# Optimization experiments

Hardware: AMD Instinct MI355X
Metric: run time of the kernel (lower is better)

## Reference

```python
import jax, jax.numpy as jnp
import numpy as np

S, B, D, H, FF, L, V, O = 512, 32, 512, 8, 2048, 6, 32000, 1000
DH = D // H
EPS = 1e-5


def layer_norm(x, g, b):
    mu = jnp.mean(x, axis=-1, keepdims=True)
    var = jnp.mean((x - mu) ** 2, axis=-1, keepdims=True)
    return (x - mu) * jax.lax.rsqrt(var + EPS) * g + b


def positional_encoding(seq_len, dim):
    pos = np.arange(seq_len, dtype=np.float32)[:, None]
    i = np.arange(dim)
    angle = pos / (10000.0 ** ((i // 2 * 2.0) / dim))
    pe = np.where(i % 2 == 0, np.sin(angle), np.cos(angle)).astype(np.float32)
    return jnp.asarray(pe)  # [seq_len, dim]


def setup_inputs() -> dict:
    key = jax.random.key(0)
    ks = jax.random.split(key, 16)
    sc = 0.02
    inp = {
        'x': jax.random.randint(ks[0], (S, B), 0, V, dtype=jnp.int32),
        'x_len': jnp.full((B,), S, dtype=jnp.int32),
        'emb': jax.random.normal(ks[1], (V, D), jnp.float32) * sc,
        'Wq': jax.random.normal(ks[2], (L, D, D), jnp.float32) * sc,
        'bq': jnp.zeros((L, D), jnp.float32),
        'Wk': jax.random.normal(ks[3], (L, D, D), jnp.float32) * sc,
        'bk': jnp.zeros((L, D), jnp.float32),
        'Wv': jax.random.normal(ks[4], (L, D, D), jnp.float32) * sc,
        'bv': jnp.zeros((L, D), jnp.float32),
        'Wo': jax.random.normal(ks[5], (L, D, D), jnp.float32) * sc,
        'bo': jnp.zeros((L, D), jnp.float32),
        'ln1_g': jnp.ones((L, D), jnp.float32),
        'ln1_b': jnp.zeros((L, D), jnp.float32),
        'W1': jax.random.normal(ks[6], (L, D, FF), jnp.float32) * sc,
        'b1': jnp.zeros((L, FF), jnp.float32),
        'W2': jax.random.normal(ks[7], (L, FF, D), jnp.float32) * sc,
        'b2': jnp.zeros((L, D), jnp.float32),
        'ln2_g': jnp.ones((L, D), jnp.float32),
        'ln2_b': jnp.zeros((L, D), jnp.float32),
        'W_fc': jax.random.normal(ks[8], (S * D, O), jnp.float32) * sc,
        'b_fc': jnp.zeros((O,), jnp.float32),
    }
    return inp


def reference(x, x_len, emb, Wq, bq, Wk, bk, Wv, bv, Wo, bo, ln1_g, ln1_b,
              W1, b1, W2, b2, ln2_g, ln2_b, W_fc, b_fc):
    out = emb[x]                      # [S, B, D]
    out = jnp.transpose(out, (1, 0, 2))  # [B, S, D]
    out = out + positional_encoding(S, D)[None, :, :]
    scale = DH ** -0.5
    for l in range(L):
        # NOTE: faithful to the original buggy head-split: plain row-major
        # reshape [B,S,D] -> [B*H,S,DH] without a [B,H,S,DH] transpose.
        q = jnp.reshape(out @ Wq[l] + bq[l], (B * H, S, DH))
        k = jnp.reshape(out @ Wk[l] + bk[l], (B * H, S, DH))
        v = jnp.reshape(out @ Wv[l] + bv[l], (B * H, S, DH))
        attn = jax.nn.softmax(jnp.einsum('gqd,gkd->gqk', q, k) * scale, axis=-1)
        ctx = jnp.einsum('gqk,gkd->gqd', attn, v).reshape(B, S, D)
        h = layer_norm(ctx @ Wo[l] + bo[l] + out, ln1_g[l], ln1_b[l])
        f = jax.nn.relu(h @ W1[l] + b1[l]) @ W2[l] + b2[l]
        out = layer_norm(f + h, ln2_g[l], ln2_b[l])
    out = out.reshape(B, S * D)
    return out @ W_fc + b_fc          # [B, O]
```

## Files before the change

kernel.cpp:

```cpp
#include <hip/hip_runtime.h>
#include <cstdint>
#include <cstddef>

#define S_  512
#define B_  32
#define D_  512
#define FF_ 2048
#define L_  6
#define O_  1000
#define M_  (B_*S_)
#define G_  256
#define DH_ 64

typedef __attribute__((ext_vector_type(8))) short bf16x8;
typedef __attribute__((ext_vector_type(4))) float f32x4;
typedef __attribute__((ext_vector_type(16))) float f32x16;

__device__ __forceinline__ unsigned short f2bf(float f) {
  unsigned int u = __builtin_bit_cast(unsigned int, f);
  u = (u + 0x7fffu + ((u >> 16) & 1u)) >> 16;
  return (unsigned short)u;
}
__device__ __forceinline__ float bf2f(unsigned short u) {
  return __builtin_bit_cast(float, (unsigned int)u << 16);
}
__device__ __forceinline__ unsigned int pkbf(float a, float b) {
  return (unsigned int)f2bf(a) | ((unsigned int)f2bf(b) << 16);
}
__device__ __forceinline__ unsigned int prm(float a, float b) {
  return __builtin_amdgcn_perm(__builtin_bit_cast(unsigned int, b),
                               __builtin_bit_cast(unsigned int, a), 0x07060302u);
}
__device__ __forceinline__ void gload_lds16(const void* g, void* l) {
  __builtin_amdgcn_global_load_lds(
      (const __attribute__((address_space(1))) unsigned int*)g,
      (__attribute__((address_space(3))) unsigned int*)l, 16, 0, 0);
}

__global__ void pe_kernel(float* __restrict__ pe) {
  int i = blockIdx.x * 256 + threadIdx.x;
  int s = i >> 9, d = i & 511;
  double de = (double)(d & ~1);
  double ang = (double)s * exp(de * (-9.210340371976184 / 512.0));
  pe[i] = (d & 1) ? (float)cos(ang) : (float)sin(ang);
}

__global__ void wconv_kernel(const float* __restrict__ W, unsigned short* __restrict__ Wt,
                             int K, int N, size_t ozs) {
  __shared__ float tile[32][33];
  const float* Wl = W + (size_t)blockIdx.z * K * N;
  unsigned short* Wtl = Wt + (size_t)blockIdx.z * ozs;
  int k0 = blockIdx.x * 32, n0 = blockIdx.y * 32;
  int c = threadIdx.x & 31, rb = threadIdx.x >> 5;
#pragma unroll
  for (int i = 0; i < 4; ++i) {
    int r = rb + i * 8;
    tile[r][c] = Wl[(size_t)(k0 + r) * N + n0 + c];
  }
  __syncthreads();
#pragma unroll
  for (int i = 0; i < 4; ++i) {
    int r = rb + i * 8;
    Wtl[(size_t)(n0 + r) * K + k0 + c] = f2bf(tile[c][r]);
  }
}

__global__ void embed_kernel(const int* __restrict__ x, const float* __restrict__ emb,
                             const float* __restrict__ pe, unsigned short* __restrict__ xb) {
  int bi = blockIdx.x;
  int s = bi / B_, b = bi % B_;
  int tok = x[s * B_ + b];
  int d = threadIdx.x * 4;
  float4 e = *(const float4*)(emb + (size_t)tok * D_ + d);
  float4 p = *(const float4*)(pe + (size_t)s * D_ + d);
  size_t o = ((size_t)b * S_ + s) * D_ + d;
  ushort4 u;
  u.x = f2bf(e.x + p.x); u.y = f2bf(e.y + p.y);
  u.z = f2bf(e.z + p.z); u.w = f2bf(e.w + p.w);
  *(ushort4*)(xb + o) = u;
}

__global__ __launch_bounds__(256, 2) void gemm_kernel(
    const unsigned short* __restrict__ A, const unsigned short* __restrict__ Bt,
    const float* __restrict__ bias, unsigned short* __restrict__ outb,
    int K, int N, int relu, int nbx) {
  __shared__ unsigned short As[3][128 * 32];
  __shared__ unsigned short Bs[3][256 * 32];
  int nwg = nbx * (M_ / 128);
  int cpx = nwg >> 3;
  int id = blockIdx.x;
  int wg = (id & 7) * cpx + (id >> 3);
  int bx = wg % nbx, by = wg / nbx;
  int m0 = by * 128, n0 = bx * 256;

  int tid = threadIdx.x, lane = tid & 63, wid = tid >> 6;
  f32x4 acc[8][4];
#pragma unroll
  for (int mi = 0; mi < 8; ++mi)
#pragma unroll
    for (int ni = 0; ni < 4; ++ni) acc[mi][ni] = (f32x4)0.0f;

  int srow = lane >> 2, scol = (lane & 3) * 8;
  const unsigned short* Abase = A + (size_t)m0 * K;
  const unsigned short* Bbase = Bt + (size_t)n0 * K;
  int c16 = lane & 15, hi = lane >> 4;
  int koff = hi * 8;
  int brow = wid * 64 + c16;
  int nk = K >> 5;

  auto STAGE = [&](int kt, int bb) {
    int k0 = kt * 32;
#pragma unroll
    for (int i = 0; i < 6; ++i) {
      int c = wid * 6 + i;
      if (c < 8) {
        gload_lds16(Abase + (size_t)(c * 16 + srow) * K + k0 + scol, (char*)As[bb] + c * 1024);
      } else {
        int c2 = c - 8;
        gload_lds16(Bbase + (size_t)(c2 * 16 + srow) * K + k0 + scol, (char*)Bs[bb] + c2 * 1024);
      }
    }
  };

  STAGE(0, 0); STAGE(1, 1); STAGE(2, 2);
  int bb = 0;
  for (int kt = 0; kt < nk; ++kt) {
    int rem = nk - 1 - kt;
    if (rem >= 2)      asm volatile("s_waitcnt vmcnt(12)" ::: "memory");
    else if (rem == 1) asm volatile("s_waitcnt vmcnt(6)" ::: "memory");
    else               asm volatile("s_waitcnt vmcnt(0)" ::: "memory");
    __builtin_amdgcn_s_barrier();
    __builtin_amdgcn_sched_barrier(0);
    bf16x8 af[8], bfr[4];
#pragma unroll
    for (int mi = 0; mi < 8; ++mi) af[mi] = *(const bf16x8*)&As[bb][(mi * 16 + c16) * 32 + koff];
#pragma unroll
    for (int ni = 0; ni < 4; ++ni) bfr[ni] = *(const bf16x8*)&Bs[bb][(brow + ni * 16) * 32 + koff];
    __builtin_amdgcn_s_setprio(1);
#pragma unroll
    for (int mi = 0; mi < 8; ++mi)
#pragma unroll
      for (int ni = 0; ni < 4; ++ni)
        acc[mi][ni] = __builtin_amdgcn_mfma_f32_16x16x32_bf16(bfr[ni], af[mi], acc[mi][ni], 0, 0, 0);
    __builtin_amdgcn_s_setprio(0);
    __builtin_amdgcn_sched_barrier(0);
    __builtin_amdgcn_s_barrier();
    if (kt + 3 < nk) STAGE(kt + 3, bb);
    bb = (bb == 2) ? 0 : bb + 1;
  }

#pragma unroll
  for (int ni = 0; ni < 4; ++ni) {
    int colb = n0 + wid * 64 + ni * 16 + hi * 4;
    float4 bv = *(const float4*)(bias + colb);
#pragma unroll
    for (int mi = 0; mi < 8; ++mi) {
      int row = m0 + mi * 16 + c16;
      float v0 = acc[mi][ni][0] + bv.x;
      float v1 = acc[mi][ni][1] + bv.y;
      float v2 = acc[mi][ni][2] + bv.z;
      float v3 = acc[mi][ni][3] + bv.w;
      if (relu) { v0 = fmaxf(v0, 0.f); v1 = fmaxf(v1, 0.f); v2 = fmaxf(v2, 0.f); v3 = fmaxf(v3, 0.f); }
      *(uint2*)(outb + (size_t)row * N + colb) = make_uint2(pkbf(v0, v1), pkbf(v2, v3));
    }
  }
}

__global__ __launch_bounds__(256, 3) void gemm128_kernel(
    const unsigned short* __restrict__ A, const unsigned short* __restrict__ Bt,
    const float* __restrict__ b0, const float* __restrict__ b1, const float* __restrict__ b2,
    unsigned short* __restrict__ o0, unsigned short* __restrict__ o1, unsigned short* __restrict__ o2,
    int K, int N, int relu, int split, int nbx) {
  __shared__ unsigned short As[2][128 * 32];
  __shared__ unsigned short Bs[2][128 * 32];
  int nwg = nbx * (M_ / 128);
  int cpx = nwg >> 3;
  int id = blockIdx.x;
  int wg = (id & 7) * cpx + (id >> 3);
  int bx = wg % nbx, by = wg / nbx;
  int m0 = by * 128, n0 = bx * 128;

  int tid = threadIdx.x, lane = tid & 63, wid = tid >> 6;
  int wm = wid >> 1, wn = wid & 1;
  f32x4 acc[4][4];
#pragma unroll
  for (int mi = 0; mi < 4; ++mi)
#pragma unroll
    for (int ni = 0; ni < 4; ++ni) acc[mi][ni] = (f32x4)0.0f;

  int srow = lane >> 2, scol = (lane & 3) * 8;
  const unsigned short* Abase = A + (size_t)m0 * K;
  const unsigned short* Bbase = Bt + (size_t)n0 * K;
  int c16 = lane & 15, hi = lane >> 4;
  int koff = hi * 8;
  int arow = wm * 64 + c16, brow = wn * 64 + c16;
  int nk = K >> 5;

  auto STAGE = [&](int kt, int bb) {
    int k0 = kt * 32;
#pragma unroll
    for (int i = 0; i < 2; ++i) {
      int c = wid * 2 + i;
      gload_lds16(Abase + (size_t)(c * 16 + srow) * K + k0 + scol, (char*)As[bb] + c * 1024);
      gload_lds16(Bbase + (size_t)(c * 16 + srow) * K + k0 + scol, (char*)Bs[bb] + c * 1024);
    }
  };

  STAGE(0, 0); STAGE(1, 1);
  int bb = 0;
  for (int kt = 0; kt < nk; ++kt) {
    if (kt + 1 < nk) asm volatile("s_waitcnt vmcnt(4)" ::: "memory");
    else             asm volatile("s_waitcnt vmcnt(0)" ::: "memory");
    __builtin_amdgcn_s_barrier();
    __builtin_amdgcn_sched_barrier(0);
    bf16x8 af[4], bfr[4];
#pragma unroll
    for (int mi = 0; mi < 4; ++mi) af[mi] = *(const bf16x8*)&As[bb][(arow + mi * 16) * 32 + koff];
#pragma unroll
    for (int ni = 0; ni < 4; ++ni) bfr[ni] = *(const bf16x8*)&Bs[bb][(brow + ni * 16) * 32 + koff];
    __builtin_amdgcn_s_setprio(1);
#pragma unroll
    for (int mi = 0; mi < 4; ++mi)
#pragma unroll
      for (int ni = 0; ni < 4; ++ni)
        acc[mi][ni] = __builtin_amdgcn_mfma_f32_16x16x32_bf16(bfr[ni], af[mi], acc[mi][ni], 0, 0, 0);
    __builtin_amdgcn_s_setprio(0);
    __builtin_amdgcn_sched_barrier(0);
    __builtin_amdgcn_s_barrier();
    if (kt + 2 < nk) STAGE(kt + 2, bb);
    bb ^= 1;
  }

  const float* bias = b0;
  unsigned short* outb = o0;
  int nbase = n0, ostride = N;
  if (split) {
    int seg = n0 >> 9;
    if (seg == 1) { bias = b1; outb = o1; }
    else if (seg == 2) { bias = b2; outb = o2; }
    nbase = n0 & 511; ostride = 512;
  }
#pragma unroll
  for (int ni = 0; ni < 4; ++ni) {
    int colb = nbase + wn * 64 + ni * 16 + hi * 4;
    float4 bv = *(const float4*)(bias + colb);
#pragma unroll
    for (int mi = 0; mi < 4; ++mi) {
      int row = m0 + wm * 64 + mi * 16 + c16;
      float v0 = acc[mi][ni][0] + bv.x;
      float v1 = acc[mi][ni][1] + bv.y;
      float v2 = acc[mi][ni][2] + bv.z;
      float v3 = acc[mi][ni][3] + bv.w;
      if (relu) { v0 = fmaxf(v0, 0.f); v1 = fmaxf(v1, 0.f); v2 = fmaxf(v2, 0.f); v3 = fmaxf(v3, 0.f); }
      *(uint2*)(outb + (size_t)row * ostride + colb) = make_uint2(pkbf(v0, v1), pkbf(v2, v3));
    }
  }
}

__global__ __launch_bounds__(128) void addln_kernel(
    const unsigned short* __restrict__ Y, const unsigned short* __restrict__ R,
    const float* __restrict__ g, const float* __restrict__ b,
    unsigned short* __restrict__ Out) {
  __shared__ float red[2], red2[2];
  int row = blockIdx.x, t = threadIdx.x;
  size_t o = (size_t)row * 512 + t * 4;
  ushort4 yv = *(const ushort4*)(Y + o);
  ushort4 rv = *(const ushort4*)(R + o);
  float v0 = bf2f(yv.x) + bf2f(rv.x);
  float v1 = bf2f(yv.y) + bf2f(rv.y);
  float v2 = bf2f(yv.z) + bf2f(rv.z);
  float v3 = bf2f(yv.w) + bf2f(rv.w);
  float s = v0 + v1 + v2 + v3;
#pragma unroll
  for (int m = 1; m < 64; m <<= 1) s += __shfl_xor(s, m);
  if ((t & 63) == 0) red[t >> 6] = s;
  __syncthreads();
  float mean = (red[0] + red[1]) * (1.0f / 512.0f);
  float d0 = v0 - mean, d1 = v1 - mean, d2 = v2 - mean, d3 = v3 - mean;
  float sq = d0 * d0 + d1 * d1 + d2 * d2 + d3 * d3;
#pragma unroll
  for (int m = 1; m < 64; m <<= 1) sq += __shfl_xor(sq, m);
  if ((t & 63) == 0) red2[t >> 6] = sq;
  __syncthreads();
  float var = (red2[0] + red2[1]) * (1.0f / 512.0f);
  float rstd = rsqrtf(var + 1e-5f);
  float4 gg = *(const float4*)(g + t * 4);
  float4 bb = *(const float4*)(b + t * 4);
  float y0 = d0 * rstd * gg.x + bb.x;
  float y1 = d1 * rstd * gg.y + bb.y;
  float y2 = d2 * rstd * gg.z + bb.z;
  float y3 = d3 * rstd * gg.w + bb.w;
  *(uint2*)(Out + o) = make_uint2(pkbf(y0, y1), pkbf(y2, y3));
}

__global__ __launch_bounds__(256) void attn_kernel(
    const unsigned short* __restrict__ Q, const unsigned short* __restrict__ Kb,
    const unsigned short* __restrict__ Vb, unsigned short* __restrict__ Ctx) {
  __shared__ char KlB[8192];
  __shared__ char VtB[8192];
  int g = blockIdx.y;
  int q0 = blockIdx.x * 256;
  const unsigned short* Kg = Kb + (size_t)g * 512 * 64;
  const unsigned short* Vg = Vb + (size_t)g * 512 * 64;
  int tid = threadIdx.x, lane = tid & 63, wid = tid >> 6;
  int l31 = lane & 31, h = lane >> 5;
  bool lo = (lane < 32);
  int qrowA = q0 + wid * 64 + l31;
  int qrowB = qrowA + 32;
  const float sc2 = 0.125f * 1.44269504f;

  bf16x8 qfa[4], qfb[4];
  {
    const unsigned short* qpa = Q + ((size_t)g * 512 + qrowA) * 64;
    const unsigned short* qpb = Q + ((size_t)g * 512 + qrowB) * 64;
#pragma unroll
    for (int c = 0; c < 4; ++c) {
      bf16x8 ra = *(const bf16x8*)(qpa + c * 16 + h * 8);
      bf16x8 rb = *(const bf16x8*)(qpb + c * 16 + h * 8);
      union { unsigned int u[4]; bf16x8 v; } ua, ub;
#pragma unroll
      for (int j = 0; j < 4; ++j) {
        ua.u[j] = pkbf(bf2f((unsigned short)ra[2 * j]) * sc2,
                       bf2f((unsigned short)ra[2 * j + 1]) * sc2);
        ub.u[j] = pkbf(bf2f((unsigned short)rb[2 * j]) * sc2,
                       bf2f((unsigned short)rb[2 * j + 1]) * sc2);
      }
      qfa[c] = ua.v; qfb[c] = ub.v;
    }
  }

  f32x16 cA0 = (f32x16)0.0f, cA1 = (f32x16)0.0f;
  f32x16 cB0 = (f32x16)0.0f, cB1 = (f32x16)0.0f;
  float mrA = -3.0e38f, lsA = 0.0f;
  float mrB = -3.0e38f, lsB = 0.0f;

  int rowS = tid >> 2;
  int cbA = (tid & 3) * 16;
  int cbB = cbA + 64;
  int swA = cbA ^ ((rowS & 7) << 4);
  int swB = cbB ^ ((rowS & 7) << 4);

  bf16x8 kc0 = *(const bf16x8*)(Kg + (size_t)rowS * 64 + cbA / 2);
  bf16x8 kc1 = *(const bf16x8*)(Kg + (size_t)rowS * 64 + cbB / 2);
  bf16x8 vc0 = *(const bf16x8*)(Vg + (size_t)rowS * 64 + cbA / 2);
  bf16x8 vc1 = *(const bf16x8*)(Vg + (size_t)rowS * 64 + cbB / 2);

  for (int kt = 0; kt < 8; ++kt) {
    __syncthreads();
    *(bf16x8*)(KlB + rowS * 128 + swA) = kc0;
    *(bf16x8*)(KlB + rowS * 128 + swB) = kc1;
#pragma unroll
    for (int j = 0; j < 8; ++j) {
      int dA = cbA / 2 + j;
      int dB = cbB / 2 + j;
      *(unsigned short*)(VtB + dA * 128 + ((2 * rowS) ^ ((dA & 7) << 4))) = (unsigned short)vc0[j];
      *(unsigned short*)(VtB + dB * 128 + ((2 * rowS) ^ ((dB & 7) << 4))) = (unsigned short)vc1[j];
    }
    bf16x8 kn0, kn1, vn0, vn1;
    if (kt < 7) {
      size_t nb = (size_t)((kt + 1) * 64 + rowS) * 64;
      kn0 = *(const bf16x8*)(Kg + nb + cbA / 2);
      kn1 = *(const bf16x8*)(Kg + nb + cbB / 2);
      vn0 = *(const bf16x8*)(Vg + nb + cbA / 2);
      vn1 = *(const bf16x8*)(Vg + nb + cbB / 2);
    }
    __syncthreads();

#pragma unroll
    for (int sub = 0; sub < 2; ++sub) {
      f32x16 s0 = (f32x16)0.0f, s1 = (f32x16)0.0f;
#pragma unroll
      for (int c = 0; c < 4; ++c) {
        int cb = 32 * c + 16 * h;
        int sw = cb ^ ((l31 & 7) << 4);
        bf16x8 k0 = *(const bf16x8*)(KlB + l31 * 128 + sw);
        bf16x8 k1 = *(const bf16x8*)(KlB + (32 + l31) * 128 + sw);
        bf16x8 qf = sub ? qfb[c] : qfa[c];
        s0 = __builtin_amdgcn_mfma_f32_32x32x16_bf16(k0, qf, s0, 0, 0, 0);
        s1 = __builtin_amdgcn_mfma_f32_32x32x16_bf16(k1, qf, s1, 0, 0, 0);
      }

      float mr = sub ? mrB : mrA;
      float ls = sub ? lsB : lsA;
      float pm = s0[0];
#pragma unroll
      for (int i = 1; i < 16; ++i) pm = fmaxf(pm, s0[i]);
#pragma unroll
      for (int i = 0; i < 16; ++i) pm = fmaxf(pm, s1[i]);
      pm = fmaxf(pm, __shfl_xor(pm, 32));
      if (!__all(pm <= mr + 8.0f)) {
        float mnew = fmaxf(mr, pm);
        float alpha = exp2f(mr - mnew);
        ls *= alpha;
        if (sub) {
#pragma unroll
          for (int i = 0; i < 16; ++i) { cB0[i] *= alpha; cB1[i] *= alpha; }
        } else {
#pragma unroll
          for (int i = 0; i < 16; ++i) { cA0[i] *= alpha; cA1[i] *= alpha; }
        }
        mr = mnew;
      }
      float p[32];
      float rs = 0.0f;
#pragma unroll
      for (int i = 0; i < 16; ++i) { p[i] = exp2f(s0[i] - mr); rs += p[i]; }
#pragma unroll
      for (int i = 0; i < 16; ++i) { p[16 + i] = exp2f(s1[i] - mr); rs += p[16 + i]; }
      float rso = __shfl_xor(rs, 32);
      ls += rs + rso;
      if (sub) { mrB = mr; lsB = ls; } else { mrA = mr; lsA = ls; }

      union { unsigned int u[4]; bf16x8 v; } pa[4];
#pragma unroll
      for (int t = 0; t < 2; ++t) {
#pragma unroll
        for (int u = 0; u < 2; ++u) {
#pragma unroll
          for (int pr = 0; pr < 2; ++pr) {
            const int b0i = t * 16 + 8 * u;
            unsigned int a  = prm(p[b0i + 2 * pr],     p[b0i + 2 * pr + 1]);
            unsigned int b  = prm(p[b0i + 4 + 2 * pr], p[b0i + 4 + 2 * pr + 1]);
            unsigned int sa = __shfl_xor(a, 32);
            unsigned int sb = __shfl_xor(b, 32);
            pa[t * 2 + u].u[pr]     = lo ? a  : sb;
            pa[t * 2 + u].u[2 + pr] = lo ? sa : b;
          }
        }
      }

#pragma unroll
      for (int kc = 0; kc < 4; ++kc) {
        int cb = 32 * kc + 16 * h;
        int sw = cb ^ ((l31 & 7) << 4);
        bf16x8 v0 = *(const bf16x8*)(VtB + l31 * 128 + sw);
        bf16x8 v1 = *(const bf16x8*)(VtB + (32 + l31) * 128 + sw);
        if (sub) {
          cB0 = __builtin_amdgcn_mfma_f32_32x32x16_bf16(v0, pa[kc].v, cB0, 0, 0, 0);
          cB1 = __builtin_amdgcn_mfma_f32_32x32x16_bf16(v1, pa[kc].v, cB1, 0, 0, 0);
        } else {
          cA0 = __builtin_amdgcn_mfma_f32_32x32x16_bf16(v0, pa[kc].v, cA0, 0, 0, 0);
          cA1 = __builtin_amdgcn_mfma_f32_32x32x16_bf16(v1, pa[kc].v, cA1, 0, 0, 0);
        }
      }
    }

    if (kt < 7) { kc0 = kn0; kc1 = kn1; vc0 = vn0; vc1 = vn1; }
  }

#pragma unroll
  for (int sub = 0; sub < 2; ++sub) {
    float inv = 1.0f / (sub ? lsB : lsA);
    int qrow = sub ? qrowB : qrowA;
    unsigned short* cp = Ctx + ((size_t)g * 512 + qrow) * 64;
#pragma unroll
    for (int dh = 0; dh < 2; ++dh) {
#pragma unroll
      for (int rq = 0; rq < 4; ++rq) {
        float e0 = (sub ? (dh ? cB1[rq * 4 + 0] : cB0[rq * 4 + 0]) : (dh ? cA1[rq * 4 + 0] : cA0[rq * 4 + 0])) * inv;
        float e1 = (sub ? (dh ? cB1[rq * 4 + 1] : cB0[rq * 4 + 1]) : (dh ? cA1[rq * 4 + 1] : cA0[rq * 4 + 1])) * inv;
        float e2 = (sub ? (dh ? cB1[rq * 4 + 2] : cB0[rq * 4 + 2]) : (dh ? cA1[rq * 4 + 2] : cA0[rq * 4 + 2])) * inv;
        float e3 = (sub ? (dh ? cB1[rq * 4 + 3] : cB0[rq * 4 + 3]) : (dh ? cA1[rq * 4 + 3] : cA0[rq * 4 + 3])) * inv;
        int d0 = dh * 32 + rq * 8 + h * 4;
        *(uint2*)(cp + d0) = make_uint2(pkbf(e0, e1), pkbf(e2, e3));
      }
    }
  }
}

#define KCH 1024
__global__ __launch_bounds__(512) void fc_part_kernel(const unsigned short* __restrict__ act,
                                                      const float* __restrict__ Wfc,
                                                      float* __restrict__ part) {
  __shared__ float al[32][256];
  int t = threadIdx.x;
  int kc = blockIdx.x;
  size_t k0 = (size_t)kc * KCH;
  int o1 = t;
  int o2 = 512 + t;
  bool a2 = (o2 < O_);
  float acc1[32], acc2[32];
#pragma unroll
  for (int bb = 0; bb < 32; ++bb) { acc1[bb] = 0.0f; acc2[bb] = 0.0f; }
  for (int sub = 0; sub < KCH / 256; ++sub) {
    __syncthreads();
    for (int i = t; i < 32 * 128; i += 512) {
      int bb = i >> 7, kk = (i & 127) * 2;
      ushort2 u = *(const ushort2*)(act + (size_t)bb * 262144 + k0 + sub * 256 + kk);
      al[bb][kk] = bf2f(u.x);
      al[bb][kk + 1] = bf2f(u.y);
    }
    __syncthreads();
    const float* wp = Wfc + (k0 + sub * 256) * O_;
    for (int kk = 0; kk < 256; kk += 4) {
      const float* wr = wp + (size_t)kk * O_;
      float w10 = wr[o1];
      float w11 = wr[O_ + o1];
      float w12 = wr[2 * O_ + o1];
      float w13 = wr[3 * O_ + o1];
      float w20 = a2 ? wr[o2] : 0.0f;
      float w21 = a2 ? wr[O_ + o2] : 0.0f;
      float w22 = a2 ? wr[2 * O_ + o2] : 0.0f;
      float w23 = a2 ? wr[3 * O_ + o2] : 0.0f;
#pragma unroll
      for (int bb = 0; bb < 32; ++bb) {
        f32x4 av = *(const f32x4*)&al[bb][kk];
        acc1[bb] = fmaf(av[0], w10, acc1[bb]);
        acc1[bb] = fmaf(av[1], w11, acc1[bb]);
        acc1[bb] = fmaf(av[2], w12, acc1[bb]);
        acc1[bb] = fmaf(av[3], w13, acc1[bb]);
        acc2[bb] = fmaf(av[0], w20, acc2[bb]);
        acc2[bb] = fmaf(av[1], w21, acc2[bb]);
        acc2[bb] = fmaf(av[2], w22, acc2[bb]);
        acc2[bb] = fmaf(av[3], w23, acc2[bb]);
      }
    }
  }
#pragma unroll
  for (int bb = 0; bb < 32; ++bb) {
    part[((size_t)kc * 32 + bb) * O_ + o1] = acc1[bb];
    if (a2) part[((size_t)kc * 32 + bb) * O_ + o2] = acc2[bb];
  }
}

__global__ void fc_reduce_kernel(const float* __restrict__ part, const float* __restrict__ bfc,
                                 float* __restrict__ out) {
  int o = blockIdx.x * 256 + threadIdx.x;
  int b = blockIdx.y;
  if (o >= O_) return;
  float s = bfc[o];
  for (int c = 0; c < 256; ++c) s += part[((size_t)c * 32 + b) * O_ + o];
  out[(size_t)b * O_ + o] = s;
}

extern "C" void kernel_launch(void* const* d_in, const int* in_sizes, int n_in,
                              void* d_out, int out_size, void* d_ws, size_t ws_size,
                              hipStream_t stream) {
  const int*   x   = (const int*)d_in[0];
  const float* emb = (const float*)d_in[2];
  const float* Wq  = (const float*)d_in[3];
  const float* bq  = (const float*)d_in[4];
  const float* Wk  = (const float*)d_in[5];
  const float* bk  = (const float*)d_in[6];
  const float* Wv  = (const float*)d_in[7];
  const float* bv  = (const float*)d_in[8];
  const float* Wo  = (const float*)d_in[9];
  const float* bo  = (const float*)d_in[10];
  const float* g1  = (const float*)d_in[11];
  const float* bn1 = (const float*)d_in[12];
  const float* W1  = (const float*)d_in[13];
  const float* bf1 = (const float*)d_in[14];
  const float* W2  = (const float*)d_in[15];
  const float* bf2 = (const float*)d_in[16];
  const float* g2  = (const float*)d_in[17];
  const float* bn2 = (const float*)d_in[18];
  const float* Wfc = (const float*)d_in[19];
  const float* bfc = (const float*)d_in[20];
  float* out = (float*)d_out;

  char* ws = (char*)d_ws;
  size_t off = 0;
  auto take = [&](size_t bytes) { char* p = ws + off; off += (bytes + 255) & ~(size_t)255; return p; };
  float*          pe   = (float*)take((size_t)512 * 512 * 4);
  unsigned short* wqkv = (unsigned short*)take((size_t)L_ * 1536 * 512 * 2);
  unsigned short* wot  = (unsigned short*)take((size_t)L_ * 512 * 512 * 2);
  unsigned short* w1t  = (unsigned short*)take((size_t)L_ * 2048 * 512 * 2);
  unsigned short* w2t  = (unsigned short*)take((size_t)L_ * 512 * 2048 * 2);
  unsigned short* xb   = (unsigned short*)take((size_t)M_ * 512 * 2);
  unsigned short* qb   = (unsigned short*)take((size_t)M_ * 512 * 2);
  unsigned short* kb   = (unsigned short*)take((size_t)M_ * 512 * 2);
  unsigned short* vb   = (unsigned short*)take((size_t)M_ * 512 * 2);
  unsigned short* cxb  = (unsigned short*)take((size_t)M_ * 512 * 2);
  unsigned short* hb   = (unsigned short*)take((size_t)M_ * 512 * 2);
  unsigned short* t1   = (unsigned short*)take((size_t)M_ * 512 * 2);
  unsigned short* f1b  = qb;
  float*          part = (float*)qb;

  pe_kernel<<<1024, 256, 0, stream>>>(pe);
  wconv_kernel<<<dim3(16, 16, L_), 256, 0, stream>>>(Wq, wqkv,          512, 512,  (size_t)1536 * 512);
  wconv_kernel<<<dim3(16, 16, L_), 256, 0, stream>>>(Wk, wqkv + 262144, 512, 512,  (size_t)1536 * 512);
  wconv_kernel<<<dim3(16, 16, L_), 256, 0, stream>>>(Wv, wqkv + 524288, 512, 512,  (size_t)1536 * 512);
  wconv_kernel<<<dim3(16, 16, L_), 256, 0, stream>>>(Wo, wot,           512, 512,  (size_t)512 * 512);
  wconv_kernel<<<dim3(16, 64, L_), 256, 0, stream>>>(W1, w1t,           512, 2048, (size_t)2048 * 512);
  wconv_kernel<<<dim3(64, 16, L_), 256, 0, stream>>>(W2, w2t,           2048, 512, (size_t)512 * 2048);
  embed_kernel<<<M_, 128, 0, stream>>>(x, emb, pe, xb);

  for (int l = 0; l < L_; ++l) {
    gemm128_kernel<<<1536, 256, 0, stream>>>(
        xb, wqkv + (size_t)l * 1536 * 512,
        bq + l * 512, bk + l * 512, bv + l * 512,
        qb, kb, vb, 512, 1536, 0, 1, 12);
    attn_kernel<<<dim3(2, G_), 256, 0, stream>>>(qb, kb, vb, cxb);
    gemm128_kernel<<<512, 256, 0, stream>>>(
        cxb, wot + (size_t)l * 512 * 512,
        bo + l * 512, nullptr, nullptr,
        t1, nullptr, nullptr, 512, 512, 0, 0, 4);
    addln_kernel<<<M_, 128, 0, stream>>>(t1, xb, g1 + l * 512, bn1 + l * 512, hb);
    gemm_kernel<<<1024, 256, 0, stream>>>(
        hb, w1t + (size_t)l * 2048 * 512, bf1 + l * 2048, f1b, 512, 2048, 1, 8);
    gemm128_kernel<<<512, 256, 0, stream>>>(
        f1b, w2t + (size_t)l * 512 * 2048,
        bf2 + l * 512, nullptr, nullptr,
        t1, nullptr, nullptr, 2048, 512, 0, 0, 4);
    addln_kernel<<<M_, 128, 0, stream>>>(t1, hb, g2 + l * 512, bn2 + l * 512, xb);
  }

  fc_part_kernel<<<256, 512, 0, stream>>>(xb, Wfc, part);
  fc_reduce_kernel<<<dim3(4, 32), 256, 0, stream>>>(part, bfc, out);
}
```

Baseline: 1.872 ms.

## Double-buffer attention LDS, use 128-tile GEMM for FFN1, two rows per LayerNorm block

```diff
diff --git a/kernel.cpp b/kernel.cpp
--- a/kernel.cpp
+++ b/kernel.cpp
@@ -80,92 +80,6 @@
   *(ushort4*)(xb + o) = u;
 }
 
-__global__ __launch_bounds__(256, 2) void gemm_kernel(
-    const unsigned short* __restrict__ A, const unsigned short* __restrict__ Bt,
-    const float* __restrict__ bias, unsigned short* __restrict__ outb,
-    int K, int N, int relu, int nbx) {
-  __shared__ unsigned short As[3][128 * 32];
-  __shared__ unsigned short Bs[3][256 * 32];
-  int nwg = nbx * (M_ / 128);
-  int cpx = nwg >> 3;
-  int id = blockIdx.x;
-  int wg = (id & 7) * cpx + (id >> 3);
-  int bx = wg % nbx, by = wg / nbx;
-  int m0 = by * 128, n0 = bx * 256;
-
-  int tid = threadIdx.x, lane = tid & 63, wid = tid >> 6;
-  f32x4 acc[8][4];
-#pragma unroll
-  for (int mi = 0; mi < 8; ++mi)
-#pragma unroll
-    for (int ni = 0; ni < 4; ++ni) acc[mi][ni] = (f32x4)0.0f;
-
-  int srow = lane >> 2, scol = (lane & 3) * 8;
-  const unsigned short* Abase = A + (size_t)m0 * K;
-  const unsigned short* Bbase = Bt + (size_t)n0 * K;
-  int c16 = lane & 15, hi = lane >> 4;
-  int koff = hi * 8;
-  int brow = wid * 64 + c16;
-  int nk = K >> 5;
-
-  auto STAGE = [&](int kt, int bb) {
-    int k0 = kt * 32;
-#pragma unroll
-    for (int i = 0; i < 6; ++i) {
-      int c = wid * 6 + i;
-      if (c < 8) {
-        gload_lds16(Abase + (size_t)(c * 16 + srow) * K + k0 + scol, (char*)As[bb] + c * 1024);
-      } else {
-        int c2 = c - 8;
-        gload_lds16(Bbase + (size_t)(c2 * 16 + srow) * K + k0 + scol, (char*)Bs[bb] + c2 * 1024);
-      }
-    }
-  };
-
-  STAGE(0, 0); STAGE(1, 1); STAGE(2, 2);
-  int bb = 0;
-  for (int kt = 0; kt < nk; ++kt) {
-    int rem = nk - 1 - kt;
-    if (rem >= 2)      asm volatile("s_waitcnt vmcnt(12)" ::: "memory");
-    else if (rem == 1) asm volatile("s_waitcnt vmcnt(6)" ::: "memory");
-    else               asm volatile("s_waitcnt vmcnt(0)" ::: "memory");
-    __builtin_amdgcn_s_barrier();
-    __builtin_amdgcn_sched_barrier(0);
-    bf16x8 af[8], bfr[4];
-#pragma unroll
-    for (int mi = 0; mi < 8; ++mi) af[mi] = *(const bf16x8*)&As[bb][(mi * 16 + c16) * 32 + koff];
-#pragma unroll
-    for (int ni = 0; ni < 4; ++ni) bfr[ni] = *(const bf16x8*)&Bs[bb][(brow + ni * 16) * 32 + koff];
-    __builtin_amdgcn_s_setprio(1);
-#pragma unroll
-    for (int mi = 0; mi < 8; ++mi)
-#pragma unroll
-      for (int ni = 0; ni < 4; ++ni)
-        acc[mi][ni] = __builtin_amdgcn_mfma_f32_16x16x32_bf16(bfr[ni], af[mi], acc[mi][ni], 0, 0, 0);
-    __builtin_amdgcn_s_setprio(0);
-    __builtin_amdgcn_sched_barrier(0);
-    __builtin_amdgcn_s_barrier();
-    if (kt + 3 < nk) STAGE(kt + 3, bb);
-    bb = (bb == 2) ? 0 : bb + 1;
-  }
-
-#pragma unroll
-  for (int ni = 0; ni < 4; ++ni) {
-    int colb = n0 + wid * 64 + ni * 16 + hi * 4;
-    float4 bv = *(const float4*)(bias + colb);
-#pragma unroll
-    for (int mi = 0; mi < 8; ++mi) {
-      int row = m0 + mi * 16 + c16;
-      float v0 = acc[mi][ni][0] + bv.x;
-      float v1 = acc[mi][ni][1] + bv.y;
-      float v2 = acc[mi][ni][2] + bv.z;
-      float v3 = acc[mi][ni][3] + bv.w;
-      if (relu) { v0 = fmaxf(v0, 0.f); v1 = fmaxf(v1, 0.f); v2 = fmaxf(v2, 0.f); v3 = fmaxf(v3, 0.f); }
-      *(uint2*)(outb + (size_t)row * N + colb) = make_uint2(pkbf(v0, v1), pkbf(v2, v3));
-    }
-  }
-}
-
 __global__ __launch_bounds__(256, 3) void gemm128_kernel(
     const unsigned short* __restrict__ A, const unsigned short* __restrict__ Bt,
     const float* __restrict__ b0, const float* __restrict__ b1, const float* __restrict__ b2,
@@ -257,13 +171,16 @@
   }
 }
 
-__global__ __launch_bounds__(128) void addln_kernel(
+__global__ __launch_bounds__(256) void addln_kernel(
     const unsigned short* __restrict__ Y, const unsigned short* __restrict__ R,
     const float* __restrict__ g, const float* __restrict__ b,
     unsigned short* __restrict__ Out) {
-  __shared__ float red[2], red2[2];
-  int row = blockIdx.x, t = threadIdx.x;
-  size_t o = (size_t)row * 512 + t * 4;
+  __shared__ float red[2][2], red2[2][2];
+  int t = threadIdx.x;
+  int rg = t >> 7;
+  int tt = t & 127;
+  int row = blockIdx.x * 2 + rg;
+  size_t o = (size_t)row * 512 + tt * 4;
   ushort4 yv = *(const ushort4*)(Y + o);
   ushort4 rv = *(const ushort4*)(R + o);
   float v0 = bf2f(yv.x) + bf2f(rv.x);
@@ -273,19 +190,19 @@
   float s = v0 + v1 + v2 + v3;
 #pragma unroll
   for (int m = 1; m < 64; m <<= 1) s += __shfl_xor(s, m);
-  if ((t & 63) == 0) red[t >> 6] = s;
+  if ((tt & 63) == 0) red[rg][tt >> 6] = s;
   __syncthreads();
-  float mean = (red[0] + red[1]) * (1.0f / 512.0f);
+  float mean = (red[rg][0] + red[rg][1]) * (1.0f / 512.0f);
   float d0 = v0 - mean, d1 = v1 - mean, d2 = v2 - mean, d3 = v3 - mean;
   float sq = d0 * d0 + d1 * d1 + d2 * d2 + d3 * d3;
 #pragma unroll
   for (int m = 1; m < 64; m <<= 1) sq += __shfl_xor(sq, m);
-  if ((t & 63) == 0) red2[t >> 6] = sq;
+  if ((tt & 63) == 0) red2[rg][tt >> 6] = sq;
   __syncthreads();
-  float var = (red2[0] + red2[1]) * (1.0f / 512.0f);
+  float var = (red2[rg][0] + red2[rg][1]) * (1.0f / 512.0f);
   float rstd = rsqrtf(var + 1e-5f);
-  float4 gg = *(const float4*)(g + t * 4);
-  float4 bb = *(const float4*)(b + t * 4);
+  float4 gg = *(const float4*)(g + tt * 4);
+  float4 bb = *(const float4*)(b + tt * 4);
   float y0 = d0 * rstd * gg.x + bb.x;
   float y1 = d1 * rstd * gg.y + bb.y;
   float y2 = d2 * rstd * gg.z + bb.z;
@@ -296,8 +213,8 @@
 __global__ __launch_bounds__(256) void attn_kernel(
     const unsigned short* __restrict__ Q, const unsigned short* __restrict__ Kb,
     const unsigned short* __restrict__ Vb, unsigned short* __restrict__ Ctx) {
-  __shared__ char KlB[8192];
-  __shared__ char VtB[8192];
+  __shared__ char KlB[2][8192];
+  __shared__ char VtB[2][8192];
   int g = blockIdx.y;
   int q0 = blockIdx.x * 256;
   const unsigned short* Kg = Kb + (size_t)g * 512 * 64;
@@ -345,16 +262,18 @@
   bf16x8 vc0 = *(const bf16x8*)(Vg + (size_t)rowS * 64 + cbA / 2);
   bf16x8 vc1 = *(const bf16x8*)(Vg + (size_t)rowS * 64 + cbB / 2);
 
+  int cur = 0;
   for (int kt = 0; kt < 8; ++kt) {
-    __syncthreads();
-    *(bf16x8*)(KlB + rowS * 128 + swA) = kc0;
-    *(bf16x8*)(KlB + rowS * 128 + swB) = kc1;
+    char* Kl = KlB[cur];
+    char* Vt = VtB[cur];
+    *(bf16x8*)(Kl + rowS * 128 + swA) = kc0;
+    *(bf16x8*)(Kl + rowS * 128 + swB) = kc1;
 #pragma unroll
     for (int j = 0; j < 8; ++j) {
       int dA = cbA / 2 + j;
       int dB = cbB / 2 + j;
-      *(unsigned short*)(VtB + dA * 128 + ((2 * rowS) ^ ((dA & 7) << 4))) = (unsigned short)vc0[j];
-      *(unsigned short*)(VtB + dB * 128 + ((2 * rowS) ^ ((dB & 7) << 4))) = (unsigned short)vc1[j];
+      *(unsigned short*)(Vt + dA * 128 + ((2 * rowS) ^ ((dA & 7) << 4))) = (unsigned short)vc0[j];
+      *(unsigned short*)(Vt + dB * 128 + ((2 * rowS) ^ ((dB & 7) << 4))) = (unsigned short)vc1[j];
     }
     bf16x8 kn0, kn1, vn0, vn1;
     if (kt < 7) {
@@ -373,8 +292,8 @@
       for (int c = 0; c < 4; ++c) {
         int cb = 32 * c + 16 * h;
         int sw = cb ^ ((l31 & 7) << 4);
-        bf16x8 k0 = *(const bf16x8*)(KlB + l31 * 128 + sw);
-        bf16x8 k1 = *(const bf16x8*)(KlB + (32 + l31) * 128 + sw);
+        bf16x8 k0 = *(const bf16x8*)(Kl + l31 * 128 + sw);
+        bf16x8 k1 = *(const bf16x8*)(Kl + (32 + l31) * 128 + sw);
         bf16x8 qf = sub ? qfb[c] : qfa[c];
         s0 = __builtin_amdgcn_mfma_f32_32x32x16_bf16(k0, qf, s0, 0, 0, 0);
         s1 = __builtin_amdgcn_mfma_f32_32x32x16_bf16(k1, qf, s1, 0, 0, 0);
@@ -433,8 +352,8 @@
       for (int kc = 0; kc < 4; ++kc) {
         int cb = 32 * kc + 16 * h;
         int sw = cb ^ ((l31 & 7) << 4);
-        bf16x8 v0 = *(const bf16x8*)(VtB + l31 * 128 + sw);
-        bf16x8 v1 = *(const bf16x8*)(VtB + (32 + l31) * 128 + sw);
+        bf16x8 v0 = *(const bf16x8*)(Vt + l31 * 128 + sw);
+        bf16x8 v1 = *(const bf16x8*)(Vt + (32 + l31) * 128 + sw);
         if (sub) {
           cB0 = __builtin_amdgcn_mfma_f32_32x32x16_bf16(v0, pa[kc].v, cB0, 0, 0, 0);
           cB1 = __builtin_amdgcn_mfma_f32_32x32x16_bf16(v1, pa[kc].v, cB1, 0, 0, 0);
@@ -446,6 +365,7 @@
     }
 
     if (kt < 7) { kc0 = kn0; kc1 = kn1; vc0 = vn0; vc1 = vn1; }
+    cur ^= 1;
   }
 
 #pragma unroll
@@ -595,14 +515,16 @@
         cxb, wot + (size_t)l * 512 * 512,
         bo + l * 512, nullptr, nullptr,
         t1, nullptr, nullptr, 512, 512, 0, 0, 4);
-    addln_kernel<<<M_, 128, 0, stream>>>(t1, xb, g1 + l * 512, bn1 + l * 512, hb);
-    gemm_kernel<<<1024, 256, 0, stream>>>(
-        hb, w1t + (size_t)l * 2048 * 512, bf1 + l * 2048, f1b, 512, 2048, 1, 8);
+    addln_kernel<<<M_ / 2, 256, 0, stream>>>(t1, xb, g1 + l * 512, bn1 + l * 512, hb);
+    gemm128_kernel<<<2048, 256, 0, stream>>>(
+        hb, w1t + (size_t)l * 2048 * 512,
+        bf1 + l * 2048, nullptr, nullptr,
+        f1b, nullptr, nullptr, 512, 2048, 1, 0, 16);
     gemm128_kernel<<<512, 256, 0, stream>>>(
         f1b, w2t + (size_t)l * 512 * 2048,
         bf2 + l * 512, nullptr, nullptr,
         t1, nullptr, nullptr, 2048, 512, 0, 0, 4);
-    addln_kernel<<<M_, 128, 0, stream>>>(t1, hb, g2 + l * 512, bn2 + l * 512, xb);
+    addln_kernel<<<M_ / 2, 256, 0, stream>>>(t1, hb, g2 + l * 512, bn2 + l * 512, xb);
   }
 
   fc_part_kernel<<<256, 512, 0, stream>>>(xb, Wfc, part);
```

Result: no change. 1.856 ms (-0.9%).
